# Kernel tuning notes

Measured on AMD Instinct MI355X. Metric: run time of the kernel, lower is better.

Reference implementation:

```python
import jax, jax.numpy as jnp
import numpy as np

DELTA_VAR = 0.5
DELTA_DIST = 1.5
ALPHA, BETA, GAMMA = 1.0, 1.0, 0.001
EPS = 1e-8


def _safe_sqrt(x):
    # sqrt with zero (sub)gradient at 0, matching torch.norm's subgradient
    pos = x > 0
    return jnp.sqrt(jnp.where(pos, x, 1.0)) * pos


def setup_inputs() -> dict:
    key = jax.random.key(0)
    k1, k2, k3 = jax.random.split(key, 3)
    B, F, H, W, K = 8, 16, 384, 384, 24
    x = jax.random.normal(k1, (B, F, H, W), dtype=jnp.float32)
    n_clusters = jax.random.randint(k2, (B,), 2, K + 1).astype(jnp.int32)
    # per-pixel instance labels, in-range per sample
    labels = jax.random.randint(k3, (B, H * W), 0, K) % n_clusters[:, None]
    target = jax.nn.one_hot(labels, K, dtype=jnp.float32)  # (B, L, K)
    target = target.transpose(0, 2, 1).reshape(B, K, H, W)
    return {"input": x, "target": target, "n_clusters": n_clusters}


def reference(input, target, n_clusters):
    B, F, H, W = input.shape
    K = target.shape[1]
    x = input.reshape(B, F, H * W)          # (b, f, l)
    t = target.reshape(B, K, H * W)         # (b, c, l)
    nc = n_clusters.astype(x.dtype)         # (b,)
    valid = (jnp.arange(K)[None, :] < n_clusters[:, None]).astype(x.dtype)  # (b, c)

    # ---- cluster means (masked segment mean; padded clusters -> 0) ----
    t_sum = t.sum(-1)                                        # (b, c)
    sums = jnp.einsum('bfl,bcl->bfc', x, t)                  # (b, f, c)
    means = sums / (t_sum[:, None, :] + EPS) * valid[:, None, :]

    # ---- variance term: ||x_l - mu_c||_2 via quadratic expansion ----
    x2 = jnp.sum(x * x, axis=1)                              # (b, l)
    m2 = jnp.sum(means * means, axis=1)                      # (b, c)
    xm = jnp.einsum('bfl,bfc->bcl', x, means)                # (b, c, l)
    d2 = jnp.maximum(x2[:, None, :] - 2.0 * xm + m2[:, :, None], 0.0)
    dist = _safe_sqrt(d2)                                    # (b, c, l)
    var = jnp.maximum(dist - DELTA_VAR, 0.0) ** 2 * t        # (b, c, l)
    c_var = var.sum(-1) / (t_sum + EPS)                      # (b, c)
    var_per = (c_var * valid).sum(-1) / (nc + EPS)
    var_term = jnp.sum(var_per * (nc > 0)) / B

    # ---- distance term: hinge on pairwise mean distances ----
    mm = jnp.einsum('bfc,bfd->bcd', means, means)            # (b, c, c)
    pd2 = jnp.maximum(m2[:, :, None] - 2.0 * mm + m2[:, None, :], 0.0)
    pdist = _safe_sqrt(pd2)                                  # (b, c, c)
    offdiag = 1.0 - jnp.eye(K, dtype=x.dtype)
    pair_mask = valid[:, :, None] * valid[:, None, :] * offdiag
    hinge = jnp.maximum(2.0 * DELTA_DIST - pdist, 0.0) ** 2 * pair_mask
    dist_per = hinge.sum((1, 2)) / (2.0 * nc * (nc - 1.0) + EPS)
    dist_term = jnp.sum(dist_per * (nc > 1)) / B

    # ---- regularization term: mean over valid clusters of ||mu_c|| ----
    norms = _safe_sqrt(m2)                                   # (b, c)
    reg_term = jnp.sum((norms * valid).sum(-1) / nc) / B

    return ALPHA * var_term + BETA * dist_term + GAMMA * reg_term
```

## Files before the change

kernel.cpp:

```cpp
#include <hip/hip_runtime.h>

#define B 8
#define F 16
#define K 24
#define L 147456
#define CHUNK1 1024
#define NCH1 (L / CHUNK1)
#define NSEG (L / 256)
#define EPSF 1e-8f
#define DELTA_VAR 0.5f
#define DELTA_DIST 1.5f
#define GAMMA 0.001f

typedef float fx4 __attribute__((ext_vector_type(4)));
typedef short bf16x8 __attribute__((ext_vector_type(8)));
typedef float f32x4 __attribute__((ext_vector_type(4)));

#define OFF_CNTP 1769472
#define OFF_VARP 1880064
#define OFF_CNT  2322432
#define OFF_VSUM 2323200
#define OFF_MEAN 2323968
#define OFF_LAB  2336256

__device__ __forceinline__ short to_bf16(float v) {
    unsigned u = __float_as_uint(v);
    return (short)((u + 0x7FFFu + ((u >> 16) & 1u)) >> 16);
}

__global__ __launch_bounds__(256) void k1_fused(const float* __restrict__ t,
                                                const float* __restrict__ x,
                                                unsigned char* __restrict__ labels,
                                                float* __restrict__ cnt_part,
                                                float* __restrict__ sum_part) {
    const int gblk = blockIdx.x;
    const int b = gblk / NCH1;
    const int ch = gblk % NCH1;
    const int tid = threadIdx.x;
    const int wave = tid >> 6;
    const int lane = tid & 63;

    __shared__ unsigned char slab[CHUNK1];
    __shared__ float hist[4][32];
    __shared__ float sacc[4][F * K];

    if (lane < 32) hist[wave][lane] = 0.f;

    const int px = ch * CHUNK1 + tid * 4;
    const fx4* t4 = (const fx4*)t;
    int lab0 = 0, lab1 = 0, lab2 = 0, lab3 = 0;
    #pragma unroll
    for (int c = 0; c < K; ++c) {
        fx4 tv = __builtin_nontemporal_load(&t4[((size_t)(b * K + c) * L + px) >> 2]);
        lab0 += c * (tv.x > 0.5f);
        lab1 += c * (tv.y > 0.5f);
        lab2 += c * (tv.z > 0.5f);
        lab3 += c * (tv.w > 0.5f);
    }
    uchar4 lv = make_uchar4((unsigned char)lab0, (unsigned char)lab1,
                            (unsigned char)lab2, (unsigned char)lab3);
    *(uchar4*)&labels[(size_t)b * L + px] = lv;
    *(uchar4*)&slab[tid * 4] = lv;
    atomicAdd(&hist[wave][lab0], 1.f);
    atomicAdd(&hist[wave][lab1], 1.f);
    atomicAdd(&hist[wave][lab2], 1.f);
    atomicAdd(&hist[wave][lab3], 1.f);
    __syncthreads();

    if (tid < K) {
        float v = hist[0][tid] + hist[1][tid] + hist[2][tid] + hist[3][tid];
        cnt_part[tid * (B * NCH1) + gblk] = v;
    }

    const int n = lane & 15;
    const int q = lane >> 4;
    f32x4 acc0 = {0.f, 0.f, 0.f, 0.f};
    f32x4 acc1 = {0.f, 0.f, 0.f, 0.f};
    const float* xr = x + (size_t)(b * F + n) * L + ch * CHUNK1 + wave * 256 + q * 8;
    const unsigned char* sl = slab + wave * 256 + q * 8;

    #pragma unroll 2
    for (int it = 0; it < 8; ++it) {
        fx4 xa = *(const fx4*)(xr + it * 32);
        fx4 xc = *(const fx4*)(xr + it * 32 + 4);
        unsigned l0 = *(const unsigned*)(sl + it * 32);
        unsigned l1 = *(const unsigned*)(sl + it * 32 + 4);

        bf16x8 afrag;
        afrag[0] = to_bf16(xa.x); afrag[1] = to_bf16(xa.y);
        afrag[2] = to_bf16(xa.z); afrag[3] = to_bf16(xa.w);
        afrag[4] = to_bf16(xc.x); afrag[5] = to_bf16(xc.y);
        afrag[6] = to_bf16(xc.z); afrag[7] = to_bf16(xc.w);

        bf16x8 bf0, bf1;
        #pragma unroll
        for (int j = 0; j < 8; ++j) {
            int lj = (j < 4) ? ((l0 >> (8 * j)) & 0xFF) : ((l1 >> (8 * (j - 4))) & 0xFF);
            bf0[j] = (lj == n)      ? (short)0x3F80 : (short)0;
            bf1[j] = (lj == n + 16) ? (short)0x3F80 : (short)0;
        }
        acc0 = __builtin_amdgcn_mfma_f32_16x16x32_bf16(afrag, bf0, acc0, 0, 0, 0);
        acc1 = __builtin_amdgcn_mfma_f32_16x16x32_bf16(afrag, bf1, acc1, 0, 0, 0);
    }

    #pragma unroll
    for (int r = 0; r < 4; ++r) {
        int f = q * 4 + r;
        sacc[wave][f * K + n] = acc0[r];
        if (n < 8) sacc[wave][f * K + 16 + n] = acc1[r];
    }
    __syncthreads();
    for (int i = tid; i < F * K; i += 256) {
        float v = sacc[0][i] + sacc[1][i] + sacc[2][i] + sacc[3][i];
        sum_part[(size_t)gblk * (F * K) + i] = v;
    }
}

__global__ __launch_bounds__(256) void k2_means(const float* __restrict__ cnt_part,
                                                const float* __restrict__ sum_part,
                                                const int* __restrict__ ncl,
                                                float* __restrict__ counts,
                                                float* __restrict__ means) {
    const int b = blockIdx.x;
    const int tid = threadIdx.x;
    __shared__ float cl[8][K];
    __shared__ float cs[K];

    if (tid < 192) {
        int c = tid >> 3, grp = tid & 7;
        const float* row = cnt_part + c * (B * NCH1) + b * NCH1 + grp * 18;
        float s = 0.f;
        #pragma unroll
        for (int j = 0; j < 18; ++j) s += row[j];
        cl[grp][c] = s;
    }
    __syncthreads();
    if (tid < K) {
        float s = 0.f;
        #pragma unroll
        for (int g = 0; g < 8; ++g) s += cl[g][tid];
        cs[tid] = s;
        counts[b * K + tid] = s;
    }
    __syncthreads();

    const int ncb = ncl[b];
    for (int r = tid; r < F * K; r += 256) {
        float s = 0.f;
        const float* base = sum_part + (size_t)b * NCH1 * (F * K) + r;
        #pragma unroll 4
        for (int j = 0; j < NCH1; ++j) s += base[(size_t)j * (F * K)];
        int c = r % K;
        float valid = (c < ncb) ? 1.f : 0.f;
        means[b * F * K + r] = s / (cs[c] + EPSF) * valid;
    }
}

__global__ __launch_bounds__(256, 2) void kc_var(const float* __restrict__ x,
                                                 const unsigned char* __restrict__ labels,
                                                 const float* __restrict__ means,
                                                 float* __restrict__ var_part) {
    const int blk = blockIdx.x;
    const int b = blk / NSEG;
    const int seg = blk % NSEG;
    const int tid = threadIdx.x;
    const int w = tid >> 6;

    __shared__ float m[F * K];
    __shared__ float vacc[4][32];

    const int l = seg * 256 + tid;
    const int lab = labels[(size_t)b * L + l];

    float xv[F];
    #pragma unroll
    for (int f = 0; f < F; ++f) xv[f] = x[(size_t)(b * F + f) * L + l];

    for (int i = tid; i < F * K; i += 256) m[i] = means[b * F * K + i];
    if ((tid & 63) < 32) vacc[w][tid & 63] = 0.f;
    __syncthreads();

    float d2 = 0.f;
    #pragma unroll
    for (int f = 0; f < F; ++f) {
        float u = xv[f] - m[f * K + lab];
        d2 += u * u;
    }
    float s = fmaxf(sqrtf(d2) - DELTA_VAR, 0.f);
    s *= s;
    atomicAdd(&vacc[w][lab], s);

    __syncthreads();
    if (tid < K) {
        float v = vacc[0][tid] + vacc[1][tid] + vacc[2][tid] + vacc[3][tid];
        var_part[tid * (B * NSEG) + blk] = v;
    }
}

__global__ __launch_bounds__(256) void kr_reduce(const float* __restrict__ part,
                                                 float* __restrict__ out) {
    const int bc = blockIdx.x;
    const int b = bc / K;
    const int c = bc % K;
    const int tid = threadIdx.x;
    const float* row = part + c * (B * NSEG) + b * NSEG;
    float s = 0.f;
    for (int j = tid; j < NSEG; j += 256) s += row[j];
    __shared__ float red[256];
    red[tid] = s;
    __syncthreads();
    for (int st = 128; st > 0; st >>= 1) {
        if (tid < st) red[tid] += red[tid + st];
        __syncthreads();
    }
    if (tid == 0) out[bc] = red[0];
}

__global__ __launch_bounds__(256) void k4_final(const float* __restrict__ means,
                                                const float* __restrict__ counts,
                                                const float* __restrict__ varsums,
                                                const int* __restrict__ ncl,
                                                float* __restrict__ out) {
    __shared__ float red[256];
    const int tid = threadIdx.x;
    float total = 0.f;
    for (int idx = tid; idx < B * K * K; idx += 256) {
        int b = idx / (K * K);
        int r = idx % (K * K);
        int c = r / K;
        int d = r % K;
        int ncb = ncl[b];
        float fnc = (float)ncb;
        if (d == 0 && c < ncb && ncb > 0) {
            float cv = varsums[b * K + c] / (counts[b * K + c] + EPSF);
            total += cv / (fnc + EPSF) * (1.0f / B);
            float m2 = 0.f;
            #pragma unroll
            for (int f = 0; f < F; ++f) {
                float mv = means[(b * F + f) * K + c];
                m2 += mv * mv;
            }
            total += GAMMA * sqrtf(m2) / fnc * (1.0f / B);
        }
        if (c != d && c < ncb && d < ncb && ncb > 1) {
            float pd2 = 0.f;
            #pragma unroll
            for (int f = 0; f < F; ++f) {
                float diff = means[(b * F + f) * K + c] - means[(b * F + f) * K + d];
                pd2 += diff * diff;
            }
            float h = fmaxf(2.f * DELTA_DIST - sqrtf(pd2), 0.f);
            total += h * h / (2.f * fnc * (fnc - 1.f) + EPSF) * (1.0f / B);
        }
    }
    red[tid] = total;
    __syncthreads();
    for (int s = 128; s > 0; s >>= 1) {
        if (tid < s) red[tid] += red[tid + s];
        __syncthreads();
    }
    if (tid == 0) out[0] = red[0];
}

extern "C" void kernel_launch(void* const* d_in, const int* in_sizes, int n_in,
                              void* d_out, int out_size, void* d_ws, size_t ws_size,
                              hipStream_t stream) {
    const float* x = (const float*)d_in[0];
    const float* t = (const float*)d_in[1];
    const int* ncl = (const int*)d_in[2];
    float* out = (float*)d_out;

    char* ws = (char*)d_ws;
    float* sum_part = (float*)ws;
    float* cnt_part = (float*)(ws + OFF_CNTP);
    float* var_part = (float*)(ws + OFF_VARP);
    float* counts   = (float*)(ws + OFF_CNT);
    float* varsums  = (float*)(ws + OFF_VSUM);
    float* means    = (float*)(ws + OFF_MEAN);
    unsigned char* labels = (unsigned char*)(ws + OFF_LAB);

    k1_fused <<<B * NCH1, 256, 0, stream>>>(t, x, labels, cnt_part, sum_part);
    k2_means <<<B, 256, 0, stream>>>(cnt_part, sum_part, ncl, counts, means);
    kc_var   <<<B * NSEG, 256, 0, stream>>>(x, labels, means, var_part);
    kr_reduce<<<B * K, 256, 0, stream>>>(var_part, varsums);
    k4_final <<<1, 256, 0, stream>>>(means, counts, varsums, ncl, out);
}
```

Measured before the change: 257.4 us.

## Fold mean and final reductions into last-block tickets, vectorize var kernel

Replaces the five-kernel pipeline with two kernels plus a memset. The last block to finish in each kernel, found through an atomic ticket, performs the means computation and the final loss reduction, which removes three small launches. The variance kernel now processes 4 pixels per thread with vector loads over 1024-pixel chunks, so it writes fewer partials. The trade-off is that the tail reductions run serially in a single block, and a memset is added to reset the tickets.

```diff
diff --git a/kernel.cpp b/kernel.cpp
--- a/kernel.cpp
+++ b/kernel.cpp
@@ -5,8 +5,8 @@
 #define K 24
 #define L 147456
 #define CHUNK1 1024
-#define NCH1 (L / CHUNK1)
-#define NSEG (L / 256)
+#define NCH1 144
+#define TOTCH 1152
 #define EPSF 1e-8f
 #define DELTA_VAR 0.5f
 #define DELTA_DIST 1.5f
@@ -18,21 +18,22 @@
 
 #define OFF_CNTP 1769472
 #define OFF_VARP 1880064
-#define OFF_CNT  2322432
-#define OFF_VSUM 2323200
-#define OFF_MEAN 2323968
-#define OFF_LAB  2336256
+#define OFF_CNT  1990656
+#define OFF_MEAN 1991424
+#define OFF_TKT  2003712
+#define OFF_LAB  2003968
 
 __device__ __forceinline__ short to_bf16(float v) {
     unsigned u = __float_as_uint(v);
     return (short)((u + 0x7FFFu + ((u >> 16) & 1u)) >> 16);
 }
 
-__global__ __launch_bounds__(256) void k1_fused(const float* __restrict__ t,
-                                                const float* __restrict__ x,
-                                                unsigned char* __restrict__ labels,
-                                                float* __restrict__ cnt_part,
-                                                float* __restrict__ sum_part) {
+__global__ __launch_bounds__(256) void k1_sums(
+        const float* __restrict__ t, const float* __restrict__ x,
+        const int* __restrict__ ncl,
+        unsigned char* __restrict__ labels, float* __restrict__ cnt_part,
+        float* __restrict__ sum_part, float* __restrict__ counts,
+        float* __restrict__ means, unsigned int* __restrict__ ticket) {
     const int gblk = blockIdx.x;
     const int b = gblk / NCH1;
     const int ch = gblk % NCH1;
@@ -66,10 +67,9 @@
     atomicAdd(&hist[wave][lab2], 1.f);
     atomicAdd(&hist[wave][lab3], 1.f);
     __syncthreads();
-
     if (tid < K) {
         float v = hist[0][tid] + hist[1][tid] + hist[2][tid] + hist[3][tid];
-        cnt_part[tid * (B * NCH1) + gblk] = v;
+        cnt_part[tid * TOTCH + gblk] = v;
     }
 
     const int n = lane & 15;
@@ -114,130 +114,118 @@
         float v = sacc[0][i] + sacc[1][i] + sacc[2][i] + sacc[3][i];
         sum_part[(size_t)gblk * (F * K) + i] = v;
     }
-}
-
-__global__ __launch_bounds__(256) void k2_means(const float* __restrict__ cnt_part,
-                                                const float* __restrict__ sum_part,
-                                                const int* __restrict__ ncl,
-                                                float* __restrict__ counts,
-                                                float* __restrict__ means) {
-    const int b = blockIdx.x;
-    const int tid = threadIdx.x;
-    __shared__ float cl[8][K];
-    __shared__ float cs[K];
-
+
+    __threadfence();
+    __shared__ bool is_last;
+    if (tid == 0) is_last = (atomicAdd(&ticket[0], 1u) == TOTCH - 1);
+    __syncthreads();
+    if (!is_last) return;
+    __threadfence();
+
+    float* cs = sacc[0];
     if (tid < 192) {
-        int c = tid >> 3, grp = tid & 7;
-        const float* row = cnt_part + c * (B * NCH1) + b * NCH1 + grp * 18;
+        int bb = tid / K, c = tid % K;
+        const float* row = cnt_part + c * TOTCH + bb * NCH1;
         float s = 0.f;
-        #pragma unroll
-        for (int j = 0; j < 18; ++j) s += row[j];
-        cl[grp][c] = s;
-    }
-    __syncthreads();
-    if (tid < K) {
+        #pragma unroll 4
+        for (int j = 0; j < NCH1; ++j) s += row[j];
+        cs[tid] = s;
+        counts[tid] = s;
+    }
+    __syncthreads();
+    for (int idx = tid; idx < B * F * K; idx += 256) {
+        int bb = idx / (F * K);
+        int r = idx % (F * K);
         float s = 0.f;
-        #pragma unroll
-        for (int g = 0; g < 8; ++g) s += cl[g][tid];
-        cs[tid] = s;
-        counts[b * K + tid] = s;
-    }
-    __syncthreads();
-
-    const int ncb = ncl[b];
-    for (int r = tid; r < F * K; r += 256) {
-        float s = 0.f;
-        const float* base = sum_part + (size_t)b * NCH1 * (F * K) + r;
+        const float* base = sum_part + (size_t)bb * NCH1 * (F * K) + r;
         #pragma unroll 4
         for (int j = 0; j < NCH1; ++j) s += base[(size_t)j * (F * K)];
         int c = r % K;
-        float valid = (c < ncb) ? 1.f : 0.f;
-        means[b * F * K + r] = s / (cs[c] + EPSF) * valid;
-    }
-}
-
-__global__ __launch_bounds__(256, 2) void kc_var(const float* __restrict__ x,
-                                                 const unsigned char* __restrict__ labels,
-                                                 const float* __restrict__ means,
-                                                 float* __restrict__ var_part) {
-    const int blk = blockIdx.x;
-    const int b = blk / NSEG;
-    const int seg = blk % NSEG;
+        float valid = (c < ncl[bb]) ? 1.f : 0.f;
+        means[idx] = s / (cs[bb * K + c] + EPSF) * valid;
+    }
+}
+
+__global__ __launch_bounds__(256) void k2_var(
+        const float* __restrict__ x, const unsigned char* __restrict__ labels,
+        const float* __restrict__ means, const float* __restrict__ counts,
+        const int* __restrict__ ncl, float* __restrict__ var_part,
+        unsigned int* __restrict__ ticket, float* __restrict__ out) {
+    const int gblk = blockIdx.x;
+    const int b = gblk / NCH1;
+    const int ch = gblk % NCH1;
     const int tid = threadIdx.x;
-    const int w = tid >> 6;
-
-    __shared__ float m[F * K];
-    __shared__ float vacc[4][32];
-
-    const int l = seg * 256 + tid;
-    const int lab = labels[(size_t)b * L + l];
-
-    float xv[F];
-    #pragma unroll
-    for (int f = 0; f < F; ++f) xv[f] = x[(size_t)(b * F + f) * L + l];
-
-    for (int i = tid; i < F * K; i += 256) m[i] = means[b * F * K + i];
-    if ((tid & 63) < 32) vacc[w][tid & 63] = 0.f;
-    __syncthreads();
-
-    float d2 = 0.f;
+    const int wave = tid >> 6;
+    const int lane = tid & 63;
+
+    __shared__ float big[3072];
+    __shared__ float hist[4][32];
+    __shared__ float vs[192], cn[192], red[256];
+
+    for (int i = tid; i < F * K; i += 256) big[i] = means[b * F * K + i];
+    if (lane < 32) hist[wave][lane] = 0.f;
+    __syncthreads();
+
+    const int px = ch * CHUNK1 + tid * 4;
+    uchar4 lv = *(const uchar4*)&labels[(size_t)b * L + px];
+    float d0 = 0.f, d1 = 0.f, d2 = 0.f, d3 = 0.f;
+    const fx4* x4 = (const fx4*)x;
     #pragma unroll
     for (int f = 0; f < F; ++f) {
-        float u = xv[f] - m[f * K + lab];
-        d2 += u * u;
-    }
-    float s = fmaxf(sqrtf(d2) - DELTA_VAR, 0.f);
-    s *= s;
-    atomicAdd(&vacc[w][lab], s);
-
+        fx4 xv = x4[((size_t)(b * F + f) * L + px) >> 2];
+        float u0 = xv.x - big[f * K + lv.x]; d0 += u0 * u0;
+        float u1 = xv.y - big[f * K + lv.y]; d1 += u1 * u1;
+        float u2 = xv.z - big[f * K + lv.z]; d2 += u2 * u2;
+        float u3 = xv.w - big[f * K + lv.w]; d3 += u3 * u3;
+    }
+    float s0 = fmaxf(sqrtf(d0) - DELTA_VAR, 0.f); s0 *= s0;
+    float s1 = fmaxf(sqrtf(d1) - DELTA_VAR, 0.f); s1 *= s1;
+    float s2 = fmaxf(sqrtf(d2) - DELTA_VAR, 0.f); s2 *= s2;
+    float s3 = fmaxf(sqrtf(d3) - DELTA_VAR, 0.f); s3 *= s3;
+    atomicAdd(&hist[wave][lv.x], s0);
+    atomicAdd(&hist[wave][lv.y], s1);
+    atomicAdd(&hist[wave][lv.z], s2);
+    atomicAdd(&hist[wave][lv.w], s3);
     __syncthreads();
     if (tid < K) {
-        float v = vacc[0][tid] + vacc[1][tid] + vacc[2][tid] + vacc[3][tid];
-        var_part[tid * (B * NSEG) + blk] = v;
-    }
-}
-
-__global__ __launch_bounds__(256) void kr_reduce(const float* __restrict__ part,
-                                                 float* __restrict__ out) {
-    const int bc = blockIdx.x;
-    const int b = bc / K;
-    const int c = bc % K;
-    const int tid = threadIdx.x;
-    const float* row = part + c * (B * NSEG) + b * NSEG;
-    float s = 0.f;
-    for (int j = tid; j < NSEG; j += 256) s += row[j];
-    __shared__ float red[256];
-    red[tid] = s;
-    __syncthreads();
-    for (int st = 128; st > 0; st >>= 1) {
-        if (tid < st) red[tid] += red[tid + st];
-        __syncthreads();
-    }
-    if (tid == 0) out[bc] = red[0];
-}
-
-__global__ __launch_bounds__(256) void k4_final(const float* __restrict__ means,
-                                                const float* __restrict__ counts,
-                                                const float* __restrict__ varsums,
-                                                const int* __restrict__ ncl,
-                                                float* __restrict__ out) {
-    __shared__ float red[256];
-    const int tid = threadIdx.x;
+        float v = hist[0][tid] + hist[1][tid] + hist[2][tid] + hist[3][tid];
+        var_part[tid * TOTCH + gblk] = v;
+    }
+
+    __threadfence();
+    __shared__ bool is_last;
+    if (tid == 0) is_last = (atomicAdd(&ticket[1], 1u) == TOTCH - 1);
+    __syncthreads();
+    if (!is_last) return;
+    __threadfence();
+
+    for (int i = tid; i < B * F * K; i += 256) big[i] = means[i];
+    if (tid < 192) {
+        int bb = tid / K, c = tid % K;
+        const float* row = var_part + c * TOTCH + bb * NCH1;
+        float s = 0.f;
+        #pragma unroll 4
+        for (int j = 0; j < NCH1; ++j) s += row[j];
+        vs[tid] = s;
+        cn[tid] = counts[tid];
+    }
+    __syncthreads();
+
     float total = 0.f;
     for (int idx = tid; idx < B * K * K; idx += 256) {
-        int b = idx / (K * K);
+        int bb = idx / (K * K);
         int r = idx % (K * K);
         int c = r / K;
         int d = r % K;
-        int ncb = ncl[b];
+        int ncb = ncl[bb];
         float fnc = (float)ncb;
         if (d == 0 && c < ncb && ncb > 0) {
-            float cv = varsums[b * K + c] / (counts[b * K + c] + EPSF);
+            float cv = vs[bb * K + c] / (cn[bb * K + c] + EPSF);
             total += cv / (fnc + EPSF) * (1.0f / B);
             float m2 = 0.f;
             #pragma unroll
             for (int f = 0; f < F; ++f) {
-                float mv = means[(b * F + f) * K + c];
+                float mv = big[(bb * F + f) * K + c];
                 m2 += mv * mv;
             }
             total += GAMMA * sqrtf(m2) / fnc * (1.0f / B);
@@ -246,7 +234,7 @@
             float pd2 = 0.f;
             #pragma unroll
             for (int f = 0; f < F; ++f) {
-                float diff = means[(b * F + f) * K + c] - means[(b * F + f) * K + d];
+                float diff = big[(bb * F + f) * K + c] - big[(bb * F + f) * K + d];
                 pd2 += diff * diff;
             }
             float h = fmaxf(2.f * DELTA_DIST - sqrtf(pd2), 0.f);
@@ -275,13 +263,14 @@
     float* cnt_part = (float*)(ws + OFF_CNTP);
     float* var_part = (float*)(ws + OFF_VARP);
     float* counts   = (float*)(ws + OFF_CNT);
-    float* varsums  = (float*)(ws + OFF_VSUM);
     float* means    = (float*)(ws + OFF_MEAN);
+    unsigned int* tickets = (unsigned int*)(ws + OFF_TKT);
     unsigned char* labels = (unsigned char*)(ws + OFF_LAB);
 
-    k1_fused <<<B * NCH1, 256, 0, stream>>>(t, x, labels, cnt_part, sum_part);
-    k2_means <<<B, 256, 0, stream>>>(cnt_part, sum_part, ncl, counts, means);
-    kc_var   <<<B * NSEG, 256, 0, stream>>>(x, labels, means, var_part);
-    kr_reduce<<<B * K, 256, 0, stream>>>(var_part, varsums);
-    k4_final <<<1, 256, 0, stream>>>(means, counts, varsums, ncl, out);
-}
+    (void)hipMemsetAsync(tickets, 0, 256, stream);
+
+    k1_sums<<<TOTCH, 256, 0, stream>>>(t, x, ncl, labels, cnt_part, sum_part,
+                                       counts, means, tickets);
+    k2_var <<<TOTCH, 256, 0, stream>>>(x, labels, means, counts, ncl,
+                                       var_part, tickets, out);
+}
```

Result: slower. 686.6 us (+166.7%).
